# Kernel optimization log

Measured on AMD Instinct MI355X. Metric: run time of the kernel, lower is better.

The kernel has to match this reference:

```python
import jax, jax.numpy as jnp
import numpy as np

T, B, E, H = 1024, 8, 1024, 16
HD = E // H                       # 64
SCALE = float(HD * 1) ** -0.5     # scaling_factor = 1


def setup_inputs() -> dict:
    key = jax.random.key(0)
    ks = jax.random.split(key, 7)
    s = 0.02
    return {
        "query": jax.random.normal(ks[0], (T, B, E), jnp.float32),
        "key_padding_mask": jax.random.bernoulli(ks[1], 0.1, (B, T)),
        "attn_bias": jax.random.normal(ks[2], (1, H, T, T), jnp.float32) * 0.1,
        "wq": jax.random.normal(ks[3], (1, E, E), jnp.float32) * s,
        "wk": jax.random.normal(ks[4], (1, E, E), jnp.float32) * s,
        "wv": jax.random.normal(ks[5], (1, E, E), jnp.float32) * s,
        "wo": jax.random.normal(ks[6], (1, E, E), jnp.float32) * s,
    }


def _group_linear(x, w):
    # x: (T, B, nb*din), w: (nb, din, dout) -> (T, B, nb*dout). nb=1 here.
    t, b, _ = x.shape
    nb, din, dout = w.shape
    y = jnp.einsum('xnd,nde->xne', x.reshape(t * b, nb, din), w)
    return y.reshape(t, b, nb * dout)


def reference(query, key_padding_mask, attn_bias, wq, wk, wv, wo):
    q = _group_linear(query, wq) * SCALE
    k = _group_linear(query, wk)
    v = _group_linear(query, wv)

    # (T, B, E) -> (B*H, T, HD), matching torch view+transpose
    def split_heads(x):
        return x.reshape(T, B * H, HD).transpose(1, 0, 2)

    q, k, v = split_heads(q), split_heads(k), split_heads(v)

    scores = jnp.einsum('bth,bsh->bts', q, k).reshape(B, H, T, T)
    scores = scores + attn_bias
    scores = jnp.where(key_padding_mask[:, None, None, :], -jnp.inf, scores)
    probs = jax.nn.softmax(scores.astype(jnp.float32), axis=-1).astype(query.dtype)

    vh = v.reshape(B, H, T, HD)  # (B*H,T,HD) -> (B,H,S,HD)
    attn = jnp.einsum('bhts,bhsd->tbhd', probs, vh).reshape(T, B, H * HD)
    return _group_linear(attn, wo)
```

## Files before the change

kernel.cpp:

```cpp
#include <hip/hip_runtime.h>


typedef __bf16 bf16x8 __attribute__((ext_vector_type(8)));
typedef float f32x4 __attribute__((ext_vector_type(4)));

#define LOG2E 1.4426950408889634f
#define QSCALE 0.18033688011112042f

static __device__ __forceinline__ unsigned short f2bf_rn(float f) {
  union { float f; unsigned u; } x;
  x.f = f;
  unsigned r = (x.u + 0x7fffu + ((x.u >> 16) & 1u)) >> 16;
  return (unsigned short)r;
}
static __device__ __forceinline__ unsigned short f2bf(float f) {
  union { float f; unsigned u; } x;
  x.f = f;
  return (unsigned short)((x.u + 0x8000u) >> 16);
}

static __device__ __forceinline__ void async_cp16(const void* g, void* l) {
  __builtin_amdgcn_global_load_lds((__attribute__((address_space(1))) void*)g,
                                   (__attribute__((address_space(3))) void*)l,
                                   16, 0, 0);
}

__global__ __launch_bounds__(256, 2) void k_prep(
    const float* __restrict__ query, const int* __restrict__ mask,
    const float* __restrict__ bias,
    const float* __restrict__ wq, const float* __restrict__ wk,
    const float* __restrict__ wv, const float* __restrict__ wo,
    unsigned short* __restrict__ Abuf, float* __restrict__ Mfg,
    unsigned short* __restrict__ WqkvT, unsigned short* __restrict__ WoT,
    unsigned short* __restrict__ B2) {
  __shared__ char shraw[128 * 132 * 2];
  const int bid = blockIdx.x;
  const int tid = threadIdx.x;

  if (bid < 1024) {
    unsigned short* tile = (unsigned short*)shraw;
    const int ss = bid & 7, tt = (bid >> 3) & 7, h = bid >> 6;
    const float* src = bias + ((long)h * 1024 + tt * 128) * 1024 + ss * 128;
#pragma unroll
    for (int c = 0; c < 16; ++c) {
      int flat = c * 256 + tid;
      int row = flat >> 5, col = (flat & 31) << 2;
      float4 v = *(const float4*)(src + (long)row * 1024 + col);
      unsigned short* t4 = &tile[row * 132 + col];
      t4[0] = f2bf_rn(v.x * LOG2E); t4[1] = f2bf_rn(v.y * LOG2E);
      t4[2] = f2bf_rn(v.z * LOG2E); t4[3] = f2bf_rn(v.w * LOG2E);
    }
    __syncthreads();
    const int wid = tid >> 6, lane = tid & 63, lanelo = lane & 15, quad = lane >> 4;
    unsigned short outv[64];
#pragma unroll
    for (int mi = 0; mi < 2; ++mi)
#pragma unroll
      for (int nj = 0; nj < 8; ++nj)
#pragma unroll
        for (int r = 0; r < 4; ++r)
          outv[mi * 32 + nj * 4 + r] =
              tile[(wid * 32 + mi * 16 + quad * 4 + r) * 132 + nj * 16 + lanelo];
    unsigned short* dst = B2 + ((((long)(h * 8 + tt) * 8 + ss) * 256 + tid) << 6);
#pragma unroll
    for (int i = 0; i < 8; ++i) ((uint4*)dst)[i] = ((const uint4*)outv)[i];
  } else if (bid < 5120) {
    float (*tile)[33] = (float(*)[33])shraw;
    const int f = bid - 1024;
    const int bx = (f & 31) << 5;
    const int by = ((f >> 5) & 31) << 5;
    const int z = f >> 10;
    const float* src = (z == 0) ? wq : (z == 1) ? wk : (z == 2) ? wv : wo;
    unsigned short* dst = (z < 3) ? WqkvT + (size_t)z * 1024 * 1024 : WoT;
    const int tx = tid & 31, ty = tid >> 5;
#pragma unroll
    for (int i = 0; i < 32; i += 8)
      tile[ty + i][tx] = src[(size_t)(by + ty + i) * 1024 + bx + tx];
    __syncthreads();
#pragma unroll
    for (int i = 0; i < 32; i += 8)
      dst[(size_t)(bx + ty + i) * 1024 + by + tx] = f2bf_rn(tile[tx][ty + i]);
  } else if (bid < 13312) {
    const int idx = (bid - 5120) * 256 + tid;
    const float4 f = ((const float4*)query)[idx];
    unsigned lo = (unsigned)f2bf_rn(f.x) | ((unsigned)f2bf_rn(f.y) << 16);
    unsigned hi = (unsigned)f2bf_rn(f.z) | ((unsigned)f2bf_rn(f.w) << 16);
    uint2 v; v.x = lo; v.y = hi;
    *(uint2*)(Abuf + (size_t)idx * 4) = v;
  } else {
    const int i = (bid - 13312) * 256 + tid;
    Mfg[i] = mask[i] ? -1e30f : 0.f;
  }
}

__global__ __launch_bounds__(512, 2) void k_gemm_qk(
    const unsigned short* __restrict__ A, const unsigned short* __restrict__ Bt,
    unsigned short* __restrict__ Qh, unsigned short* __restrict__ Kh) {
  __shared__ unsigned short smem[65536];

  const int tid = threadIdx.x;
  const int wid = tid >> 6;
  const int lane = tid & 63;
  const int lanelo = lane & 15;
  const int quad = lane >> 4;
  const int wm = (wid >> 2) << 7;
  const int wn = (wid & 3) << 6;
  const int K = 1024;

  const int flat = blockIdx.y * 8 + blockIdx.x;
  const int swz = (flat & 7) * 32 + (flat >> 3);
  const int bx = swz & 7, by = swz >> 3;
  const long m0 = (long)by * 256;
  const long n0 = (long)bx * 256;

  const int x_ = (tid & 7) ^ ((tid >> 3) & 7);
  const int row_s = ((tid >> 3) << 1) + (x_ >> 2);
  const int col_s = (x_ & 3) << 3;
  const unsigned short* gA = A + (m0 + row_s) * K + col_s;
  const unsigned short* gB = Bt + (n0 + row_s) * K + col_s;

#define STG(slot, gp, kc)                                        \
  do {                                                           \
    const unsigned short* _g = (gp) + (kc);                      \
    char* _l = (char*)smem + ((slot) << 14) + (wid << 10);       \
    async_cp16(_g, _l);                                          \
    async_cp16(_g + 128 * 1024, _l + 8192);                      \
  } while (0)

  const int lhalf = lanelo >> 1;
  const int posa = ((((lanelo & 1) << 2) + quad) ^ lhalf) << 3;
  const int aoff = ((wm >> 1) + lhalf) * 64 + posa;
  const int boff = ((wn >> 1) + lhalf) * 64 + posa;

  bf16x8 a[4], b[4];
#define LDA4(slot, mb)                                                        \
  do {                                                                        \
    a[0] = *(const bf16x8*)(smem + (slot) * 8192 + aoff + ((mb) + 0) * 512);  \
    a[1] = *(const bf16x8*)(smem + (slot) * 8192 + aoff + ((mb) + 1) * 512);  \
    a[2] = *(const bf16x8*)(smem + (slot) * 8192 + aoff + ((mb) + 2) * 512);  \
    a[3] = *(const bf16x8*)(smem + (slot) * 8192 + aoff + ((mb) + 3) * 512);  \
  } while (0)
#define LDB4(slot)                                                            \
  do {                                                                        \
    b[0] = *(const bf16x8*)(smem + (slot) * 8192 + boff + 0 * 512);           \
    b[1] = *(const bf16x8*)(smem + (slot) * 8192 + boff + 1 * 512);           \
    b[2] = *(const bf16x8*)(smem + (slot) * 8192 + boff + 2 * 512);           \
    b[3] = *(const bf16x8*)(smem + (slot) * 8192 + boff + 3 * 512);           \
  } while (0)

  f32x4 acc[8][4];
  const f32x4 z4 = {0.f, 0.f, 0.f, 0.f};
#pragma unroll
  for (int i = 0; i < 8; ++i)
#pragma unroll
    for (int j = 0; j < 4; ++j) acc[i][j] = z4;

#define MMA16(mb)                                                             \
  do {                                                                        \
    __builtin_amdgcn_s_setprio(1);                                            \
    _Pragma("unroll") for (int x = 0; x < 4; ++x)                             \
        _Pragma("unroll") for (int y = 0; y < 4; ++y)                         \
        acc[(mb) + x][y] = __builtin_amdgcn_mfma_f32_16x16x32_bf16(           \
            a[x], b[y], acc[(mb) + x][y], 0, 0, 0);                           \
    __builtin_amdgcn_s_setprio(0);                                            \
  } while (0)

#define BARSYNC()                                                             \
  do {                                                                        \
    __builtin_amdgcn_s_barrier();                                             \
    __builtin_amdgcn_sched_barrier(0);                                        \
  } while (0)

  STG(2, gB, 0);
  STG(0, gA, 0);
  STG(3, gB, 32);
  STG(1, gA, 32);
  STG(6, gB, 64);
  STG(4, gA, 64);
  STG(7, gB, 96);
  asm volatile("s_waitcnt vmcnt(6)" ::: "memory");
  BARSYNC();

#pragma unroll 1
  for (int i = 0; i < 7; ++i) {
    const int kc1 = i * 128 + 96;
    const int kc2 = i * 128 + 128;
    const int kc3 = i * 128 + 192;
    LDA4(0, 0);
    LDB4(2);
    STG(5, gA, kc1);
    BARSYNC();
    MMA16(0);
    BARSYNC();
    LDA4(0, 4);
    STG(2, gB, kc2);
    BARSYNC();
    MMA16(4);
    BARSYNC();
    LDA4(1, 0);
    LDB4(3);
    STG(0, gA, kc2);
    BARSYNC();
    MMA16(0);
    BARSYNC();
    LDA4(1, 4);
    STG(3, gB, kc2 + 32);
    BARSYNC();
    MMA16(4);
    asm volatile("s_waitcnt vmcnt(6)" ::: "memory");
    BARSYNC();
    LDA4(4, 0);
    LDB4(6);
    STG(1, gA, kc2 + 32);
    BARSYNC();
    MMA16(0);
    BARSYNC();
    LDA4(4, 4);
    STG(6, gB, kc3);
    BARSYNC();
    MMA16(4);
    BARSYNC();
    LDA4(5, 0);
    LDB4(7);
    STG(4, gA, kc3);
    BARSYNC();
    MMA16(0);
    BARSYNC();
    LDA4(5, 4);
    STG(7, gB, kc3 + 32);
    BARSYNC();
    MMA16(4);
    asm volatile("s_waitcnt vmcnt(6)" ::: "memory");
    BARSYNC();
  }
  {
    LDA4(0, 0);
    LDB4(2);
    STG(5, gA, 7 * 128 + 96);
    BARSYNC();
    MMA16(0);
    BARSYNC();
    LDA4(0, 4);
    BARSYNC();
    MMA16(4);
    BARSYNC();
    LDA4(1, 0);
    LDB4(3);
    BARSYNC();
    MMA16(0);
    BARSYNC();
    LDA4(1, 4);
    BARSYNC();
    MMA16(4);
    asm volatile("s_waitcnt vmcnt(0)" ::: "memory");
    BARSYNC();
    LDA4(4, 0);
    LDB4(6);
    BARSYNC();
    MMA16(0);
    BARSYNC();
    LDA4(4, 4);
    BARSYNC();
    MMA16(4);
    BARSYNC();
    LDA4(5, 0);
    LDB4(7);
    BARSYNC();
    MMA16(0);
    BARSYNC();
    LDA4(5, 4);
    BARSYNC();
    MMA16(4);
  }
#undef STG
#undef LDA4
#undef LDB4
#undef MMA16
#undef BARSYNC

  const int which = bx >> 2;
#pragma unroll
  for (int mi = 0; mi < 8; ++mi)
#pragma unroll
    for (int nj = 0; nj < 4; ++nj)
#pragma unroll
      for (int r = 0; r < 4; ++r) {
        int m = (int)m0 + wm + mi * 16 + quad * 4 + r;
        int n = (int)n0 + wn + nj * 16 + lanelo;
        float v = acc[mi][nj][r];
        int t = m >> 3, bb = m & 7;
        int e = n & 1023, h = e >> 6, d = e & 63;
        long off = ((long)(bb * 16 + h)) << 16;
        if (which == 0)
          Qh[off + t * 64 + d] = f2bf(v * QSCALE);
        else
          Kh[off + t * 64 + d] = f2bf(v);
      }
}

static __device__ __forceinline__ void gemm_tile_128x128(
    const unsigned short* __restrict__ A, const unsigned short* __restrict__ Bt,
    int K, long m0, long n0,
    unsigned short* As, unsigned short* Bs, f32x4 acc[4][4]) {
  const int tid = threadIdx.x;
  const int wid = tid >> 6;
  const int lane = tid & 63;
  const int lanelo = lane & 15;
  const int quad = lane >> 4;
  const int wm = (wid >> 1) << 6;
  const int wn = (wid & 1) << 6;
  const int srow = tid >> 3;
  const int scol = (((tid & 7) ^ (srow & 7)) << 3);

  for (int k0 = 0; k0 < K; k0 += 64) {
    __syncthreads();
    {
      char* la = (char*)As + (wid << 10);
      char* lb = (char*)Bs + (wid << 10);
#pragma unroll
      for (int c = 0; c < 4; ++c) {
        const unsigned short* ga = A + (m0 + srow + c * 32) * K + k0 + scol;
        const unsigned short* gb = Bt + (n0 + srow + c * 32) * K + k0 + scol;
        async_cp16(ga, la + c * 4096);
        async_cp16(gb, lb + c * 4096);
      }
    }
    __syncthreads();
#pragma unroll
    for (int kk = 0; kk < 2; ++kk) {
      bf16x8 a[4], b[4];
#pragma unroll
      for (int i = 0; i < 4; ++i) {
        const int ra = wm + i * 16 + lanelo;
        const int rb = wn + i * 16 + lanelo;
        a[i] = *(const bf16x8*)(As + ra * 64 + (((kk * 4 + quad) ^ (ra & 7)) << 3));
        b[i] = *(const bf16x8*)(Bs + rb * 64 + (((kk * 4 + quad) ^ (rb & 7)) << 3));
      }
#pragma unroll
      for (int i = 0; i < 4; ++i)
#pragma unroll
        for (int j = 0; j < 4; ++j)
          acc[i][j] = __builtin_amdgcn_mfma_f32_16x16x32_bf16(a[i], b[j], acc[i][j], 0, 0, 0);
    }
  }
}

__global__ __launch_bounds__(256, 2) void k_gemm_v(
    const unsigned short* __restrict__ A, const unsigned short* __restrict__ Bt,
    unsigned short* __restrict__ Vt) {
  __shared__ unsigned short smem[16384];
  unsigned short* As = smem;
  unsigned short* Bs = smem + 8192;
  f32x4 acc[4][4];
  const f32x4 z4 = {0.f, 0.f, 0.f, 0.f};
#pragma unroll
  for (int i = 0; i < 4; ++i)
#pragma unroll
    for (int j = 0; j < 4; ++j) acc[i][j] = z4;

  const int flat = blockIdx.y * 8 + blockIdx.x;
  const int swz = (flat & 7) * 64 + (flat >> 3);
  const long m0 = (long)(swz / 8) * 128;
  const long n0 = 2048 + (long)(swz % 8) * 128;
  gemm_tile_128x128(A, Bt, 1024, m0, n0, As, Bs, acc);

  const int tid = threadIdx.x;
  const int wid = tid >> 6;
  const int lane = tid & 63;
  const int lanelo = lane & 15;
  const int quad = lane >> 4;
  const int wm = (wid >> 1) << 6;
  const int wn = (wid & 1) << 6;

  unsigned short* Vt_s = smem;
  const long t0g = m0 >> 3;
#pragma unroll
  for (int half = 0; half < 2; ++half) {
    __syncthreads();
    if ((wid & 1) == half) {
#pragma unroll
      for (int mi = 0; mi < 4; ++mi)
#pragma unroll
        for (int nj = 0; nj < 4; ++nj)
#pragma unroll
          for (int r = 0; r < 4; ++r)
            Vt_s[(wm + mi * 16 + quad * 4 + r) * 72 + nj * 16 + lanelo] =
                f2bf(acc[mi][nj][r]);
    }
    __syncthreads();
    const int h = (((int)(n0 & 1023)) >> 6) + half;
#pragma unroll
    for (int pp = 0; pp < 2; ++pp) {
      int p = tid + pp * 256;
      int b = p >> 6, d = p & 63;
      long off = ((long)(b * 16 + h)) << 16;
      __attribute__((aligned(16))) unsigned short vals[16];
#pragma unroll
      for (int t = 0; t < 16; ++t) vals[t] = Vt_s[(t * 8 + b) * 72 + d];
      uint4* dst = (uint4*)(Vt + off + (long)d * 1024 + t0g);
      dst[0] = ((const uint4*)vals)[0];
      dst[1] = ((const uint4*)vals)[1];
    }
  }
}

__global__ __launch_bounds__(512, 4) void k_attn(
    const unsigned short* __restrict__ Qh, const unsigned short* __restrict__ Kh,
    const unsigned short* __restrict__ Vt, const unsigned short* __restrict__ B2,
    const float* __restrict__ Mfg, unsigned short* __restrict__ A2) {
  __shared__ unsigned short Ks[128 * 72];
  __shared__ unsigned short Vs[64 * 136];
  __shared__ unsigned short Ps[128 * 72];

  const int tid = threadIdx.x;
  const int wid = tid >> 6;
  const int lane = tid & 63;
  const int lanelo = lane & 15;
  const int quad = lane >> 4;
  const int bh = blockIdx.x;
  const int b = bh >> 4, h = bh & 15;
  const int tt = blockIdx.y;
  const int t0 = tt * 128;
  const long head = (long)bh << 16;

  bf16x8 aq[2];
#pragma unroll
  for (int ks = 0; ks < 2; ++ks)
    aq[ks] = *(const bf16x8*)(Qh + head +
                              (long)(t0 + wid * 16 + lanelo) * 64 +
                              ks * 32 + quad * 8);

  const f32x4 z4 = {0.f, 0.f, 0.f, 0.f};
  f32x4 Oacc[4];
#pragma unroll
  for (int dj = 0; dj < 4; ++dj) Oacc[dj] = z4;
  float mrow[4], lrow[4];
#pragma unroll
  for (int r = 0; r < 4; ++r) { mrow[r] = -1e30f; lrow[r] = 0.f; }

  const long biasbase = (((long)(h * 8 + tt) * 8) * 256 + (wid >> 1) * 64 + lane) * 64 +
                        (wid & 1) * 32;

  for (int s0 = 0; s0 < 1024; s0 += 128) {
    bf16x8 bfr[4];
    {
      const bf16x8* bp8 = (const bf16x8*)(B2 + biasbase + ((long)(s0 >> 7) * 256 << 6));
#pragma unroll
      for (int i = 0; i < 4; ++i) bfr[i] = bp8[i];
    }
    float madd[8];
#pragma unroll
    for (int nj = 0; nj < 8; ++nj)
      madd[nj] = Mfg[(long)b * 1024 + s0 + nj * 16 + lanelo];

    __syncthreads();
#pragma unroll
    for (int c = 0; c < 2; ++c) {
      int flat = c * 4096 + tid * 8;
      int row = flat >> 6, col = flat & 63;
      uint4 v = *(const uint4*)(Kh + head + (long)(s0 + row) * 64 + col);
      *(uint4*)&Ks[row * 72 + col] = v;
    }
#pragma unroll
    for (int c = 0; c < 2; ++c) {
      int flat = c * 4096 + tid * 8;
      int row = flat >> 7, col = flat & 127;
      uint4 v = *(const uint4*)(Vt + head + (long)row * 1024 + s0 + col);
      *(uint4*)&Vs[row * 136 + col] = v;
    }
    __syncthreads();

    f32x4 S[8];
#pragma unroll
    for (int nj = 0; nj < 8; ++nj)
#pragma unroll
      for (int r = 0; r < 4; ++r)
        S[nj][r] = (float)bfr[nj >> 1][(nj & 1) * 4 + r] + madd[nj];

#pragma unroll
    for (int ks = 0; ks < 2; ++ks) {
      bf16x8 bk[8];
#pragma unroll
      for (int nj = 0; nj < 8; ++nj)
        bk[nj] = *(const bf16x8*)(Ks + (nj * 16 + lanelo) * 72 + ks * 32 + quad * 8);
#pragma unroll
      for (int nj = 0; nj < 8; ++nj)
        S[nj] = __builtin_amdgcn_mfma_f32_16x16x32_bf16(aq[ks], bk[nj], S[nj], 0, 0, 0);
    }

#pragma unroll
    for (int r = 0; r < 4; ++r) {
      float mx = S[0][r];
#pragma unroll
      for (int nj = 1; nj < 8; ++nj) mx = fmaxf(mx, S[nj][r]);
      mx = fmaxf(mx, __shfl_xor(mx, 1, 16));
      mx = fmaxf(mx, __shfl_xor(mx, 2, 16));
      mx = fmaxf(mx, __shfl_xor(mx, 4, 16));
      mx = fmaxf(mx, __shfl_xor(mx, 8, 16));
      float mold = mrow[r];
      float mnew = fmaxf(mold, mx);
      float al = exp2f(mold - mnew);
      mrow[r] = mnew;
      float rs = 0.f;
#pragma unroll
      for (int nj = 0; nj < 8; ++nj) {
        float p = exp2f(S[nj][r] - mnew);
        S[nj][r] = p;
        rs += p;
      }
      rs += __shfl_xor(rs, 1, 16);
      rs += __shfl_xor(rs, 2, 16);
      rs += __shfl_xor(rs, 4, 16);
      rs += __shfl_xor(rs, 8, 16);
      lrow[r] = lrow[r] * al + rs;
#pragma unroll
      for (int dj = 0; dj < 4; ++dj) Oacc[dj][r] *= al;
    }

#pragma unroll
    for (int half = 0; half < 2; ++half) {
#pragma unroll
      for (int njl = 0; njl < 4; ++njl)
#pragma unroll
        for (int r = 0; r < 4; ++r)
          Ps[(wid * 16 + quad * 4 + r) * 72 + njl * 16 + lanelo] =
              f2bf(S[half * 4 + njl][r]);
#pragma unroll
      for (int ks2 = 0; ks2 < 2; ++ks2) {
        const int ks = half * 2 + ks2;
        bf16x8 ap, bv[4];
        ap = *(const bf16x8*)(Ps + (wid * 16 + lanelo) * 72 + ks2 * 32 + quad * 8);
#pragma unroll
        for (int dj = 0; dj < 4; ++dj)
          bv[dj] = *(const bf16x8*)(Vs + (dj * 16 + lanelo) * 136 + ks * 32 + quad * 8);
#pragma unroll
        for (int dj = 0; dj < 4; ++dj)
          Oacc[dj] = __builtin_amdgcn_mfma_f32_16x16x32_bf16(ap, bv[dj], Oacc[dj], 0, 0, 0);
      }
    }
  }

#pragma unroll
  for (int r = 0; r < 4; ++r) {
    float rinv = __builtin_amdgcn_rcpf(lrow[r]);
    int t = t0 + wid * 16 + quad * 4 + r;
#pragma unroll
    for (int dj = 0; dj < 4; ++dj) {
      int d = dj * 16 + lanelo;
      A2[(long)(t * 8 + b) * 1024 + h * 64 + d] = f2bf(Oacc[dj][r] * rinv);
    }
  }
}

__global__ __launch_bounds__(256, 2) void k_gemm_out(
    const unsigned short* __restrict__ A, const unsigned short* __restrict__ Bt,
    float* __restrict__ out) {
  __shared__ unsigned short As[128 * 64];
  __shared__ unsigned short Bs[128 * 64];
  f32x4 acc[4][4];
  const f32x4 z4 = {0.f, 0.f, 0.f, 0.f};
#pragma unroll
  for (int i = 0; i < 4; ++i)
#pragma unroll
    for (int j = 0; j < 4; ++j) acc[i][j] = z4;

  const int flat = blockIdx.y * 8 + blockIdx.x;
  const int swz = (flat & 7) * 64 + (flat >> 3);
  const long m0 = (long)(swz / 8) * 128;
  const long n0 = (long)(swz % 8) * 128;
  gemm_tile_128x128(A, Bt, 1024, m0, n0, As, Bs, acc);

  const int tid = threadIdx.x;
  const int wid = tid >> 6;
  const int lane = tid & 63;
  const int lanelo = lane & 15;
  const int quad = lane >> 4;
  const int wm = (wid >> 1) << 6;
  const int wn = (wid & 1) << 6;
#pragma unroll
  for (int mi = 0; mi < 4; ++mi)
#pragma unroll
    for (int nj = 0; nj < 4; ++nj)
#pragma unroll
      for (int r = 0; r < 4; ++r) {
        long m = m0 + wm + mi * 16 + quad * 4 + r;
        long n = n0 + wn + nj * 16 + lanelo;
        out[m * 1024 + n] = acc[mi][nj][r];
      }
}

extern "C" void kernel_launch(void* const* d_in, const int* in_sizes, int n_in,
                              void* d_out, int out_size, void* d_ws, size_t ws_size,
                              hipStream_t stream) {
  const float* query = (const float*)d_in[0];
  const int* mask = (const int*)d_in[1];
  const float* bias = (const float*)d_in[2];
  const float* wq = (const float*)d_in[3];
  const float* wk = (const float*)d_in[4];
  const float* wv = (const float*)d_in[5];
  const float* wo = (const float*)d_in[6];
  float* out = (float*)d_out;

  char* ws = (char*)d_ws;
  const size_t MB = 1024 * 1024;
  unsigned short* Abuf  = (unsigned short*)(ws);
  unsigned short* WqkvT = (unsigned short*)(ws + 16 * MB);
  unsigned short* WoT   = (unsigned short*)(ws + 22 * MB);
  unsigned short* Qh    = (unsigned short*)(ws + 24 * MB);
  unsigned short* Kh    = (unsigned short*)(ws + 40 * MB);
  unsigned short* Vt    = (unsigned short*)(ws + 56 * MB);
  unsigned short* A2    = (unsigned short*)(ws + 72 * MB);
  unsigned short* B2    = (unsigned short*)(ws + 88 * MB);
  float*          Mfg   = (float*)(ws + 120 * MB);

  k_prep<<<dim3(13344), dim3(256), 0, stream>>>(query, mask, bias, wq, wk, wv, wo,
                                                Abuf, Mfg, WqkvT, WoT, B2);
  k_gemm_qk<<<dim3(8, 32), dim3(512), 0, stream>>>(Abuf, WqkvT, Qh, Kh);
  k_gemm_v<<<dim3(8, 64), dim3(256), 0, stream>>>(Abuf, WqkvT, Vt);
  k_attn<<<dim3(128, 8), dim3(512), 0, stream>>>(Qh, Kh, Vt, B2, Mfg, A2);
  k_gemm_out<<<dim3(8, 64), dim3(256), 0, stream>>>(A2, WoT, out);
}
```

Before: 350.5 us.

## Fuse V projection into the 256x256 QK GEMM kernel

Extends the QK projection GEMM grid from 8 to 12 column tiles so V columns are computed by the same optimized 256x256 pipelined kernel. The separate 128x128 V GEMM launch is removed. V tiles get a transposing epilogue through shared memory, writing 32 time steps per thread per head. This drops one launch, lets V use the better-tuned large-tile GEMM, and gives a single 384-block wave. The cost is an epilogue with four barrier-separated passes.

```diff
diff --git a/kernel.cpp b/kernel.cpp
--- a/kernel.cpp
+++ b/kernel.cpp
@@ -93,9 +93,10 @@
   }
 }
 
-__global__ __launch_bounds__(512, 2) void k_gemm_qk(
+__global__ __launch_bounds__(512, 2) void k_gemm_qkv(
     const unsigned short* __restrict__ A, const unsigned short* __restrict__ Bt,
-    unsigned short* __restrict__ Qh, unsigned short* __restrict__ Kh) {
+    unsigned short* __restrict__ Qh, unsigned short* __restrict__ Kh,
+    unsigned short* __restrict__ Vt) {
   __shared__ unsigned short smem[65536];
 
   const int tid = threadIdx.x;
@@ -107,9 +108,9 @@
   const int wn = (wid & 3) << 6;
   const int K = 1024;
 
-  const int flat = blockIdx.y * 8 + blockIdx.x;
-  const int swz = (flat & 7) * 32 + (flat >> 3);
-  const int bx = swz & 7, by = swz >> 3;
+  const int flat = blockIdx.y * 12 + blockIdx.x;
+  const int swz = (flat & 7) * 48 + (flat >> 3);
+  const int bx = swz % 12, by = swz / 12;
   const long m0 = (long)by * 256;
   const long n0 = (long)bx * 256;
 
@@ -279,23 +280,55 @@
 #undef BARSYNC
 
   const int which = bx >> 2;
-#pragma unroll
-  for (int mi = 0; mi < 8; ++mi)
-#pragma unroll
-    for (int nj = 0; nj < 4; ++nj)
-#pragma unroll
-      for (int r = 0; r < 4; ++r) {
-        int m = (int)m0 + wm + mi * 16 + quad * 4 + r;
-        int n = (int)n0 + wn + nj * 16 + lanelo;
-        float v = acc[mi][nj][r];
-        int t = m >> 3, bb = m & 7;
-        int e = n & 1023, h = e >> 6, d = e & 63;
-        long off = ((long)(bb * 16 + h)) << 16;
-        if (which == 0)
-          Qh[off + t * 64 + d] = f2bf(v * QSCALE);
-        else
-          Kh[off + t * 64 + d] = f2bf(v);
+  if (which < 2) {
+#pragma unroll
+    for (int mi = 0; mi < 8; ++mi)
+#pragma unroll
+      for (int nj = 0; nj < 4; ++nj)
+#pragma unroll
+        for (int r = 0; r < 4; ++r) {
+          int m = (int)m0 + wm + mi * 16 + quad * 4 + r;
+          int n = (int)n0 + wn + nj * 16 + lanelo;
+          float v = acc[mi][nj][r];
+          int t = m >> 3, bb = m & 7;
+          int e = n & 1023, h = e >> 6, d = e & 63;
+          long off = ((long)(bb * 16 + h)) << 16;
+          if (which == 0)
+            Qh[off + t * 64 + d] = f2bf(v * QSCALE);
+          else
+            Kh[off + t * 64 + d] = f2bf(v);
+        }
+  } else {
+    unsigned short* Vt_s = smem;
+    const long t0g = m0 >> 3;
+    const int bb = wid;
+    const int d = lane;
+#pragma unroll
+    for (int qn = 0; qn < 4; ++qn) {
+      __syncthreads();
+      if ((wid & 3) == qn) {
+#pragma unroll
+        for (int mi = 0; mi < 8; ++mi)
+#pragma unroll
+          for (int nj = 0; nj < 4; ++nj)
+#pragma unroll
+            for (int r = 0; r < 4; ++r)
+              Vt_s[(wm + mi * 16 + quad * 4 + r) * 72 + nj * 16 + lanelo] =
+                  f2bf(acc[mi][nj][r]);
       }
+      __syncthreads();
+      const int h = (int)(((n0 + qn * 64) & 1023) >> 6);
+      long off = ((long)(bb * 16 + h)) << 16;
+      __attribute__((aligned(16))) unsigned short vals[32];
+#pragma unroll
+      for (int t = 0; t < 32; ++t) vals[t] = Vt_s[(t * 8 + bb) * 72 + d];
+      uint4* dst = (uint4*)(Vt + off + (long)d * 1024 + t0g);
+      dst[0] = ((const uint4*)vals)[0];
+      dst[1] = ((const uint4*)vals)[1];
+      dst[2] = ((const uint4*)vals)[2];
+      dst[3] = ((const uint4*)vals)[3];
+    }
+  }
 }
 
 static __device__ __forceinline__ void gemm_tile_128x128(
@@ -345,65 +378,6 @@
   }
 }
 
-__global__ __launch_bounds__(256, 2) void k_gemm_v(
-    const unsigned short* __restrict__ A, const unsigned short* __restrict__ Bt,
-    unsigned short* __restrict__ Vt) {
-  __shared__ unsigned short smem[16384];
-  unsigned short* As = smem;
-  unsigned short* Bs = smem + 8192;
-  f32x4 acc[4][4];
-  const f32x4 z4 = {0.f, 0.f, 0.f, 0.f};
-#pragma unroll
-  for (int i = 0; i < 4; ++i)
-#pragma unroll
-    for (int j = 0; j < 4; ++j) acc[i][j] = z4;
-
-  const int flat = blockIdx.y * 8 + blockIdx.x;
-  const int swz = (flat & 7) * 64 + (flat >> 3);
-  const long m0 = (long)(swz / 8) * 128;
-  const long n0 = 2048 + (long)(swz % 8) * 128;
-  gemm_tile_128x128(A, Bt, 1024, m0, n0, As, Bs, acc);
-
-  const int tid = threadIdx.x;
-  const int wid = tid >> 6;
-  const int lane = tid & 63;
-  const int lanelo = lane & 15;
-  const int quad = lane >> 4;
-  const int wm = (wid >> 1) << 6;
-  const int wn = (wid & 1) << 6;
-
-  unsigned short* Vt_s = smem;
-  const long t0g = m0 >> 3;
-#pragma unroll
-  for (int half = 0; half < 2; ++half) {
-    __syncthreads();
-    if ((wid & 1) == half) {
-#pragma unroll
-      for (int mi = 0; mi < 4; ++mi)
-#pragma unroll
-        for (int nj = 0; nj < 4; ++nj)
-#pragma unroll
-          for (int r = 0; r < 4; ++r)
-            Vt_s[(wm + mi * 16 + quad * 4 + r) * 72 + nj * 16 + lanelo] =
-                f2bf(acc[mi][nj][r]);
-    }
-    __syncthreads();
-    const int h = (((int)(n0 & 1023)) >> 6) + half;
-#pragma unroll
-    for (int pp = 0; pp < 2; ++pp) {
-      int p = tid + pp * 256;
-      int b = p >> 6, d = p & 63;
-      long off = ((long)(b * 16 + h)) << 16;
-      __attribute__((aligned(16))) unsigned short vals[16];
-#pragma unroll
-      for (int t = 0; t < 16; ++t) vals[t] = Vt_s[(t * 8 + b) * 72 + d];
-      uint4* dst = (uint4*)(Vt + off + (long)d * 1024 + t0g);
-      dst[0] = ((const uint4*)vals)[0];
-      dst[1] = ((const uint4*)vals)[1];
-    }
-  }
-}
-
 __global__ __launch_bounds__(512, 4) void k_attn(
     const unsigned short* __restrict__ Qh, const unsigned short* __restrict__ Kh,
     const unsigned short* __restrict__ Vt, const unsigned short* __restrict__ B2,
@@ -615,8 +589,7 @@
 
   k_prep<<<dim3(13344), dim3(256), 0, stream>>>(query, mask, bias, wq, wk, wv, wo,
                                                 Abuf, Mfg, WqkvT, WoT, B2);
-  k_gemm_qk<<<dim3(8, 32), dim3(512), 0, stream>>>(Abuf, WqkvT, Qh, Kh);
-  k_gemm_v<<<dim3(8, 64), dim3(256), 0, stream>>>(Abuf, WqkvT, Vt);
+  k_gemm_qkv<<<dim3(12, 32), dim3(512), 0, stream>>>(Abuf, WqkvT, Qh, Kh, Vt);
   k_attn<<<dim3(128, 8), dim3(512), 0, stream>>>(Qh, Kh, Vt, B2, Mfg, A2);
   k_gemm_out<<<dim3(8, 64), dim3(256), 0, stream>>>(A2, WoT, out);
 }
```

Measured after the change: 358.9 us. 2.4% more time.
